# Performance work log

Measured on AMD Instinct MI355X. Metric: run time of the kernel, lower is better.

## Reference

```python
import jax, jax.numpy as jnp
import numpy as np

T, B, D_IN, H, V = 512, 128, 1024, 128, 4
NH, HD, MAXLEN = 4, 32, 64  # 4 heads * 32 = embed_dim 128; MAX_LENGTH=64


def _cell(pre, h, c, Whh):
    # pre = x @ W_ih.T + b, computed by caller. PyTorch gate order: i, f, g, o.
    g = pre + h @ Whh.T
    i, f, gg, o = jnp.split(g, 4, axis=-1)
    c = jax.nn.sigmoid(f) * c + jax.nn.sigmoid(i) * jnp.tanh(gg)
    h = jax.nn.sigmoid(o) * jnp.tanh(c)
    return h, c


def _lstm_layer(xs, Wih, Whh, b):
    # xs: [T, B, D]; input GEMM hoisted out of the scan as one big matmul
    pre = xs @ Wih.T + b  # [T, B, 4H]
    z = jnp.zeros((xs.shape[1], Whh.shape[1]), xs.dtype)

    def step(carry, p):
        h, c = carry
        h, c = _cell(p, h, c, Whh)
        return (h, c), h

    _, hs = jax.lax.scan(step, (z, z), pre)
    return hs  # [T, B, H]


def setup_inputs() -> dict:
    key = jax.random.key(0)
    ks = jax.random.split(key, 23)
    s = 0.08

    def rn(k, shape):
        return jax.random.normal(k, shape, jnp.float32) * s

    return {
        "x": jax.random.normal(ks[0], (T, B, D_IN), jnp.float32),
        "enc_Wih0": rn(ks[1], (4 * H, D_IN)), "enc_Whh0": rn(ks[2], (4 * H, H)), "enc_b0": rn(ks[3], (4 * H,)),
        "enc_Wih1": rn(ks[4], (4 * H, H)), "enc_Whh1": rn(ks[5], (4 * H, H)), "enc_b1": rn(ks[6], (4 * H,)),
        "dec_Wih0": rn(ks[7], (4 * H, H + V)), "dec_Whh0": rn(ks[8], (4 * H, H)), "dec_b0": rn(ks[9], (4 * H,)),
        "dec_Wih1": rn(ks[10], (4 * H, H)), "dec_Whh1": rn(ks[11], (4 * H, H)), "dec_b1": rn(ks[12], (4 * H,)),
        "Wq": rn(ks[13], (H, H)), "bq": rn(ks[14], (H,)),
        "Wk": rn(ks[15], (H, H)), "bk": rn(ks[16], (H,)),
        "Wv": rn(ks[17], (H, H)), "bv": rn(ks[18], (H,)),
        "Wo": rn(ks[19], (H, H)), "bo": rn(ks[20], (H,)),
        "lin_W": rn(ks[21], (V, 2 * H)), "lin_b": rn(ks[22], (V,)),
    }


def reference(x, enc_Wih0, enc_Whh0, enc_b0, enc_Wih1, enc_Whh1, enc_b1,
              dec_Wih0, dec_Whh0, dec_b0, dec_Wih1, dec_Whh1, dec_b1,
              Wq, bq, Wk, bk, Wv, bv, Wo, bo, lin_W, lin_b):
    # 2-layer encoder LSTM over the CNN feature sequence
    enc = _lstm_layer(_lstm_layer(x, enc_Wih0, enc_Whh0, enc_b0),
                      enc_Wih1, enc_Whh1, enc_b1)  # [T, B, H]

    # K/V projections of the (fixed) encoding hoisted out of the decode loop
    k = (enc @ Wk.T + bk).reshape(T, B, NH, HD)
    v = (enc @ Wv.T + bv).reshape(T, B, NH, HD)
    scale = 1.0 / float(np.sqrt(HD))

    z = jnp.zeros((B, H), x.dtype)

    def step(carry, _):
        h0, c0, h1, c1, y, ct = carry
        xin = jnp.concatenate([y, ct], axis=-1)  # cat([y, c_t]) -> [B, V+H]
        h0, c0 = _cell(xin @ dec_Wih0.T + dec_b0, h0, c0, dec_Whh0)
        h1, c1 = _cell(h0 @ dec_Wih1.T + dec_b1, h1, c1, dec_Whh1)
        s1 = h1  # top-layer LSTM output, query of length 1
        q = (s1 @ Wq.T + bq).reshape(B, NH, HD)
        attn = jax.nn.softmax(jnp.einsum('bhd,tbhd->bht', q, k) * scale, axis=-1)
        ct = jnp.einsum('bht,tbhd->bhd', attn, v).reshape(B, H) @ Wo.T + bo
        y = jnp.concatenate([s1, ct], axis=-1) @ lin_W.T + lin_b  # [B, V]
        return (h0, c0, h1, c1, y, ct), y

    init = (z, z, z, z, jnp.zeros((B, V), x.dtype), z)
    _, ys = jax.lax.scan(step, init, None, length=MAXLEN)
    return ys  # [MAX_LENGTH, B, V]
```

## Files before the change

### kernel.cpp

```cpp
#include <hip/hip_runtime.h>
#include <hip/hip_bf16.h>

typedef __attribute__((ext_vector_type(8))) short s16x8;
typedef __attribute__((ext_vector_type(4))) float f32x4;

__device__ inline unsigned short f2bf(float f) {
  unsigned u = __builtin_bit_cast(unsigned, f);
  unsigned r = (u + 0x7FFFu + ((u >> 16) & 1u)) >> 16;
  return (unsigned short)r;
}
__device__ inline float bf2f(short v) {
  return __builtin_bit_cast(float, ((unsigned)(unsigned short)v) << 16);
}
__device__ inline float bflo(unsigned w) { return __builtin_bit_cast(float, w << 16); }
__device__ inline float bfhi(unsigned w) { return __builtin_bit_cast(float, w & 0xFFFF0000u); }
__device__ inline float sigf(float x) { return 1.f / (1.f + __expf(-x)); }
__device__ inline float tanhf_(float x) { float e = __expf(2.f * x); return 1.f - 2.f / (e + 1.f); }

__global__ void packT(const float* __restrict__ src, unsigned* __restrict__ dst,
                      int rows, int scols, int kkPairs) {
  int i = blockIdx.x * 256 + threadIdx.x;
  if (i >= kkPairs * rows) return;
  int kk = i / rows, o = i % rows;
  int k0 = 2 * kk, k1 = 2 * kk + 1;
  float lo = (k0 < scols) ? src[(size_t)o * scols + k0] : 0.f;
  float hi = (k1 < scols) ? src[(size_t)o * scols + k1] : 0.f;
  dst[i] = (unsigned)f2bf(lo) | ((unsigned)f2bf(hi) << 16);
}
__global__ void packTg(const float* __restrict__ src, unsigned* __restrict__ dst,
                       int scols, int kkPairs) {
  int i = blockIdx.x * 256 + threadIdx.x;
  if (i >= kkPairs * 512) return;
  int kk = i / 512, j = i % 512;
  int row = (j & 3) * 128 + (j >> 2);
  int k0 = 2 * kk, k1 = 2 * kk + 1;
  float lo = (k0 < scols) ? src[(size_t)row * scols + k0] : 0.f;
  float hi = (k1 < scols) ? src[(size_t)row * scols + k1] : 0.f;
  dst[i] = (unsigned)f2bf(lo) | ((unsigned)f2bf(hi) << 16);
}
__global__ void f2bf_vec(const float* __restrict__ src, unsigned short* __restrict__ dst) {
  size_t i = ((size_t)blockIdx.x * 256 + threadIdx.x) * 4;
  float4 v = *(const float4*)(src + i);
  ushort4 o;
  o.x = f2bf(v.x); o.y = f2bf(v.y); o.z = f2bf(v.z); o.w = f2bf(v.w);
  *(ushort4*)(dst + i) = o;
}

#define BM 128
#define BN 128
#define BKK 32

template<int A_BF16, int C_BF16>
__global__ __launch_bounds__(256) void gemm_bt(const void* __restrict__ Av,
    const float* __restrict__ B, const float* __restrict__ bias,
    void* __restrict__ Cv, int M, int N, int K) {
  __shared__ short sA[BM * BKK];
  __shared__ short sB[BN * BKK];
  const int tid = threadIdx.x;
  const int l = tid & 63;
  const int wid = tid >> 6;
  const int wr = wid >> 1, wc = wid & 1;
  const int lr = l & 15, kg = l >> 4;
  const int bn = blockIdx.x, bm = blockIdx.y;
  const int arow = tid >> 1;
  const int acol = (tid & 1) * 16;

  f32x4 acc[4][4];
#pragma unroll
  for (int i = 0; i < 4; ++i)
#pragma unroll
    for (int j = 0; j < 4; ++j) acc[i][j] = (f32x4){0.f, 0.f, 0.f, 0.f};

  for (int kt = 0; kt < K; kt += BKK) {
    __syncthreads();
    if (A_BF16) {
      const unsigned short* src = (const unsigned short*)Av + (size_t)(bm * BM + arow) * K + kt + acol;
      *(s16x8*)&sA[arow * BKK + acol] = *(const s16x8*)src;
      *(s16x8*)&sA[arow * BKK + acol + 8] = *(const s16x8*)(src + 8);
    } else {
      const float* src = (const float*)Av + (size_t)(bm * BM + arow) * K + kt + acol;
      s16x8 v0, v1;
#pragma unroll
      for (int e = 0; e < 8; ++e) { v0[e] = (short)f2bf(src[e]); v1[e] = (short)f2bf(src[8 + e]); }
      *(s16x8*)&sA[arow * BKK + acol] = v0;
      *(s16x8*)&sA[arow * BKK + acol + 8] = v1;
    }
    {
      const float* src = B + (size_t)(bn * BN + arow) * K + kt + acol;
      s16x8 v0, v1;
#pragma unroll
      for (int e = 0; e < 8; ++e) { v0[e] = (short)f2bf(src[e]); v1[e] = (short)f2bf(src[8 + e]); }
      *(s16x8*)&sB[arow * BKK + acol] = v0;
      *(s16x8*)&sB[arow * BKK + acol + 8] = v1;
    }
    __syncthreads();
    s16x8 af[4], bfr[4];
#pragma unroll
    for (int mi = 0; mi < 4; ++mi)
      af[mi] = *(const s16x8*)&sA[(wr * 64 + mi * 16 + lr) * BKK + kg * 8];
#pragma unroll
    for (int ni = 0; ni < 4; ++ni)
      bfr[ni] = *(const s16x8*)&sB[(wc * 64 + ni * 16 + lr) * BKK + kg * 8];
#pragma unroll
    for (int mi = 0; mi < 4; ++mi)
#pragma unroll
      for (int ni = 0; ni < 4; ++ni)
        acc[mi][ni] = __builtin_amdgcn_mfma_f32_16x16x32_bf16(af[mi], bfr[ni], acc[mi][ni], 0, 0, 0);
  }
  const int r0 = bm * BM + wr * 64;
  const int c0 = bn * BN + wc * 64;
#pragma unroll
  for (int mi = 0; mi < 4; ++mi)
#pragma unroll
    for (int ni = 0; ni < 4; ++ni) {
      const int col = c0 + ni * 16 + lr;
      const float bv = bias[col];
#pragma unroll
      for (int e = 0; e < 4; ++e) {
        const int row = r0 + mi * 16 + kg * 4 + e;
        const float v = acc[mi][ni][e] + bv;
        if (C_BF16) ((unsigned short*)Cv)[(size_t)row * N + col] = f2bf(v);
        else        ((float*)Cv)[(size_t)row * N + col] = v;
      }
    }
}

__global__ __launch_bounds__(512) void lstm_scan(const float* __restrict__ pre,
    const float* __restrict__ Whh, unsigned short* __restrict__ hs, int T) {
  __shared__ unsigned short hb[2][2048];
  const int tid = threadIdx.x;
  const int l = tid & 63, w = tid >> 6;
  const int wg = blockIdx.x;
  const int lr = l & 15, kg = l >> 4;
  const int col = w * 16 + lr;
  const int rbase = kg * 4;

  s16x8 wf[4][4];
#pragma unroll
  for (int gi = 0; gi < 4; ++gi)
#pragma unroll
    for (int kk = 0; kk < 4; ++kk) {
      const float* p = Whh + (size_t)(gi * 128 + col) * 128 + kk * 32 + kg * 8;
#pragma unroll
      for (int e = 0; e < 8; ++e) wf[gi][kk][e] = (short)f2bf(p[e]);
    }
  for (int i = tid; i < 4096; i += 512) ((unsigned short*)hb)[i] = 0;
  float c[4] = {0.f, 0.f, 0.f, 0.f};

  const float* pbase = pre + ((size_t)(wg * 16 + rbase)) * 512 + col;
  float pf[16];
#pragma unroll
  for (int gi = 0; gi < 4; ++gi)
#pragma unroll
    for (int e = 0; e < 4; ++e) pf[gi * 4 + e] = pbase[e * 512 + gi * 128];
  __syncthreads();

  for (int t = 0; t < T; ++t) {
    const unsigned short* hc = hb[t & 1];
    unsigned short* hn = hb[(t & 1) ^ 1];
    s16x8 a[4];
#pragma unroll
    for (int kk = 0; kk < 4; ++kk) {
      const int byt = lr * 256 + ((kk * 64 + kg * 16) ^ ((lr & 7) << 4));
      a[kk] = *(const s16x8*)((const char*)hc + byt);
    }
    f32x4 acc[4];
#pragma unroll
    for (int gi = 0; gi < 4; ++gi)
      acc[gi] = (f32x4){pf[gi * 4], pf[gi * 4 + 1], pf[gi * 4 + 2], pf[gi * 4 + 3]};
    float pfn[16];
    if (t + 1 < T) {
      const float* pb2 = pbase + (size_t)(t + 1) * 65536;
#pragma unroll
      for (int gi = 0; gi < 4; ++gi)
#pragma unroll
        for (int e = 0; e < 4; ++e) pfn[gi * 4 + e] = pb2[e * 512 + gi * 128];
    } else {
#pragma unroll
      for (int i2 = 0; i2 < 16; ++i2) pfn[i2] = 0.f;
    }
#pragma unroll
    for (int kk = 0; kk < 4; ++kk)
#pragma unroll
      for (int gi = 0; gi < 4; ++gi)
        acc[gi] = __builtin_amdgcn_mfma_f32_16x16x32_bf16(a[kk], wf[gi][kk], acc[gi], 0, 0, 0);
#pragma unroll
    for (int e = 0; e < 4; ++e) {
      float gi_ = sigf(acc[0][e]);
      float gf  = sigf(acc[1][e]);
      float gg  = tanhf_(acc[2][e]);
      float go  = sigf(acc[3][e]);
      c[e] = gf * c[e] + gi_ * gg;
      float h = go * tanhf_(c[e]);
      unsigned short hu = f2bf(h);
      int row = rbase + e;
      int byt = row * 256 + ((col * 2) ^ ((row & 7) << 4));
      *(unsigned short*)((char*)hn + byt) = hu;
      hs[((size_t)t * 128 + wg * 16 + row) * 128 + col] = hu;
    }
#pragma unroll
    for (int i2 = 0; i2 < 16; ++i2) pf[i2] = pfn[i2];
    __syncthreads();
  }
}


#define DEC_SMEM 147200

__global__ void __launch_bounds__(512, 1) decoder_single(
    const unsigned short* __restrict__ kb, const unsigned short* __restrict__ vb,
    const unsigned* __restrict__ w0t,  const unsigned* __restrict__ wh0t,
    const unsigned* __restrict__ wi1t, const unsigned* __restrict__ wh1t,
    const unsigned* __restrict__ wqt,  const unsigned* __restrict__ wot,
    const float* __restrict__ b0, const float* __restrict__ b1,
    const float* __restrict__ bq, const float* __restrict__ bo,
    const float* __restrict__ linW, const float* __restrict__ linb,
    float* __restrict__ out)
{
  extern __shared__ char smem[];
  unsigned short* Kl = (unsigned short*)smem;
  float* xin = (float*)(smem + 131072);
  float* h0p = (float*)(smem + 131648);
  float* h1p = (float*)(smem + 132672);
  float* qx  = (float*)(smem + 133696);
  float* ctv = (float*)(smem + 134208);
  float* sc  = (float*)(smem + 134720);
  float* avp = (float*)(smem + 142912);
  float* part= (float*)(smem + 144960);
  float* red = (float*)(smem + 147008);
  float* isl = (float*)(smem + 147136);

  const int b = blockIdx.x;
  const int tid = threadIdx.x;
  const int l = tid & 63, wv = tid >> 6;
  const int lb = l & ~3;
  const int gate = tid & 3, o512 = tid >> 2;
  const int o128 = tid & 127, qd = tid >> 7;

  {
    const unsigned* kb32 = (const unsigned*)kb;
#pragma unroll
    for (int it = 0; it < 64; ++it) {
      const int i = tid + it * 512;
      const int t = i >> 6, c32 = i & 63;
      const unsigned v = kb32[(size_t)t * 8192 + b * 64 + c32];
      const int slot = c32 >> 2, w32 = c32 & 3;
      *(unsigned*)((char*)Kl + t * 256 + (((slot + t) & 15) << 4) + w32 * 4) = v;
    }
  }
  const float b0r = b0[gate * 128 + o512];
  const float b1r = b1[gate * 128 + o512];
  const float bqr = bq[o128];
  const float bor = bo[o128];
  float cc0 = 0.f, cc1 = 0.f;

  if (tid < 136) xin[tid] = 0.f;
  if (tid < 128) { h0p[tid] = 0.f; h0p[128 + tid] = 0.f; h1p[tid] = 0.f; h1p[128 + tid] = 0.f; }
  __syncthreads();

  const float scale = 0.1767766952966369f;

  for (int s = 0; s < 64; ++s) {
    const float* h0c = h0p + (s & 1) * 128;
    float* h0n = h0p + ((s & 1) ^ 1) * 128;
    const float* h1c = h1p + (s & 1) * 128;
    float* h1n = h1p + ((s & 1) ^ 1) * 128;

    {
      float a0 = b0r, a1 = 0.f;
      const unsigned* wp = w0t + tid;
#pragma unroll 8
      for (int kk = 0; kk < 68; ++kk) {
        const unsigned w2 = wp[kk * 512];
        const float2 x2 = *(const float2*)(xin + 2 * kk);
        a0 += x2.x * bflo(w2); a1 += x2.y * bfhi(w2);
      }
      const unsigned* hp = wh0t + tid;
#pragma unroll 8
      for (int kk = 0; kk < 64; ++kk) {
        const unsigned w2 = hp[kk * 512];
        const float2 h2 = *(const float2*)(h0c + 2 * kk);
        a0 += h2.x * bflo(w2); a1 += h2.y * bfhi(w2);
      }
      const float gval = a0 + a1;
      const float iv = __shfl(gval, lb + 0);
      const float fv = __shfl(gval, lb + 1);
      const float gv = __shfl(gval, lb + 2);
      const float ov = __shfl(gval, lb + 3);
      cc0 = sigf(fv) * cc0 + sigf(iv) * tanhf_(gv);
      const float h = sigf(ov) * tanhf_(cc0);
      if (gate == 0) h0n[o512] = h;
    }
    __syncthreads();
    {
      float a0 = b1r, a1 = 0.f;
      const unsigned* ip = wi1t + tid;
      const unsigned* hp = wh1t + tid;
#pragma unroll 8
      for (int kk = 0; kk < 64; ++kk) {
        const unsigned wa = ip[kk * 512];
        const unsigned wb = hp[kk * 512];
        const float2 a2 = *(const float2*)(h0n + 2 * kk);
        const float2 b2 = *(const float2*)(h1c + 2 * kk);
        a0 += a2.x * bflo(wa) + b2.x * bflo(wb);
        a1 += a2.y * bfhi(wa) + b2.y * bfhi(wb);
      }
      const float gval = a0 + a1;
      const float iv = __shfl(gval, lb + 0);
      const float fv = __shfl(gval, lb + 1);
      const float gv = __shfl(gval, lb + 2);
      const float ov = __shfl(gval, lb + 3);
      cc1 = sigf(fv) * cc1 + sigf(iv) * tanhf_(gv);
      const float h = sigf(ov) * tanhf_(cc1);
      if (gate == 0) h1n[o512] = h;
    }
    __syncthreads();
    {
      float a0 = 0.f, a1 = 0.f;
      const unsigned* wp = wqt + (size_t)(qd * 16) * 128 + o128;
#pragma unroll
      for (int m = 0; m < 16; ++m) {
        const unsigned w2 = wp[(size_t)m * 128];
        const float2 h2 = *(const float2*)(h1n + qd * 32 + 2 * m);
        a0 += h2.x * bflo(w2);
        a1 += h2.y * bfhi(w2);
      }
      part[qd * 128 + o128] = a0 + a1;
    }
    __syncthreads();
    if (tid < 128)
      qx[tid] = (bqr + part[tid] + part[128 + tid] + part[256 + tid] + part[384 + tid]) * scale;
    __syncthreads();
    {
      const int t = tid;
      float s0 = 0.f, s1 = 0.f, s2 = 0.f, s3 = 0.f;
      const char* krow = (const char*)Kl + t * 256;
#pragma unroll
      for (int c = 0; c < 16; ++c) {
        const s16x8 kv = *(const s16x8*)(krow + (((c + t) & 15) << 4));
        const f32x4 qA = *(const f32x4*)(qx + c * 8);
        const f32x4 qB = *(const f32x4*)(qx + c * 8 + 4);
        float d = qA[0] * bf2f(kv[0]) + qA[1] * bf2f(kv[1]) + qA[2] * bf2f(kv[2]) + qA[3] * bf2f(kv[3])
                + qB[0] * bf2f(kv[4]) + qB[1] * bf2f(kv[5]) + qB[2] * bf2f(kv[6]) + qB[3] * bf2f(kv[7]);
        if ((c >> 2) == 0) s0 += d; else if ((c >> 2) == 1) s1 += d; else if ((c >> 2) == 2) s2 += d; else s3 += d;
      }
      float p0 = __expf(s0), p1 = __expf(s1), p2 = __expf(s2), p3 = __expf(s3);
      sc[0 * 512 + t] = p0; sc[1 * 512 + t] = p1; sc[2 * 512 + t] = p2; sc[3 * 512 + t] = p3;
#pragma unroll
      for (int off = 32; off > 0; off >>= 1) {
        p0 += __shfl_xor(p0, off); p1 += __shfl_xor(p1, off);
        p2 += __shfl_xor(p2, off); p3 += __shfl_xor(p3, off);
      }
      if (l == 0) { red[0 + wv] = p0; red[8 + wv] = p1; red[16 + wv] = p2; red[24 + wv] = p3; }
    }
    __syncthreads();
    if (tid < 4) {
      float sm = red[tid * 8];
#pragma unroll
      for (int w2 = 1; w2 < 8; ++w2) sm += red[tid * 8 + w2];
      isl[tid] = 1.f / sm;
    }
    {
      const int d = tid & 127, tc = tid >> 7, h = d >> 5;
      const unsigned short* vp = vb + (size_t)(tc * 128) * 16384 + (size_t)b * 128 + d;
      const float* scp = sc + h * 512 + tc * 128;
      float acc = 0.f;
#pragma unroll 8
      for (int tt = 0; tt < 128; ++tt)
        acc += scp[tt] * bf2f((short)vp[(size_t)tt * 16384]);
      avp[tc * 128 + d] = acc;
    }
    __syncthreads();
    if (tid < 128)
      ctv[tid] = (avp[tid] + avp[128 + tid] + avp[256 + tid] + avp[384 + tid]) * isl[tid >> 5];
    __syncthreads();
    {
      float a0 = 0.f, a1 = 0.f;
      const unsigned* wp = wot + (size_t)(qd * 16) * 128 + o128;
#pragma unroll
      for (int m = 0; m < 16; ++m) {
        const unsigned w2 = wp[(size_t)m * 128];
        const float2 c2 = *(const float2*)(ctv + qd * 32 + 2 * m);
        a0 += c2.x * bflo(w2);
        a1 += c2.y * bfhi(w2);
      }
      part[qd * 128 + o128] = a0 + a1;
    }
    __syncthreads();
    if (tid < 128)
      xin[4 + tid] = bor + part[tid] + part[128 + tid] + part[256 + tid] + part[384 + tid];
    __syncthreads();
    if (tid < 256) {
      const int o = tid >> 6, j = tid & 63;
      const float* lw = linW + o * 256;
      float p = h1n[j] * lw[j] + h1n[j + 64] * lw[j + 64]
              + xin[4 + j] * lw[128 + j] + xin[4 + j + 64] * lw[192 + j];
#pragma unroll
      for (int off = 32; off > 0; off >>= 1) p += __shfl_xor(p, off);
      if (j == 0) {
        const float yv = p + linb[o];
        out[((size_t)s * 128 + b) * 4 + o] = yv;
        xin[o] = yv;
      }
    }
    __syncthreads();
  }
}

extern "C" void kernel_launch(void* const* d_in, const int* in_sizes, int n_in,
                              void* d_out, int out_size, void* d_ws, size_t ws_size,
                              hipStream_t stream) {
  (void)in_sizes; (void)n_in; (void)out_size;
  const float* x     = (const float*)d_in[0];
  const float* eWih0 = (const float*)d_in[1];
  const float* eWhh0 = (const float*)d_in[2];
  const float* eb0   = (const float*)d_in[3];
  const float* eWih1 = (const float*)d_in[4];
  const float* eWhh1 = (const float*)d_in[5];
  const float* eb1   = (const float*)d_in[6];
  const float* dWih0 = (const float*)d_in[7];
  const float* dWhh0 = (const float*)d_in[8];
  const float* db0   = (const float*)d_in[9];
  const float* dWih1 = (const float*)d_in[10];
  const float* dWhh1 = (const float*)d_in[11];
  const float* db1   = (const float*)d_in[12];
  const float* Wq    = (const float*)d_in[13];
  const float* bq    = (const float*)d_in[14];
  const float* Wk    = (const float*)d_in[15];
  const float* bk    = (const float*)d_in[16];
  const float* Wv    = (const float*)d_in[17];
  const float* bv    = (const float*)d_in[18];
  const float* Wo    = (const float*)d_in[19];
  const float* bo    = (const float*)d_in[20];
  const float* linW  = (const float*)d_in[21];
  const float* linb  = (const float*)d_in[22];

  char* w = (char*)d_ws;
  float* pre  = (float*)(w + 524288);
  size_t off = 524288 + (size_t)65536 * 512 * 4;
  unsigned short* hs0  = (unsigned short*)(w + off); off += (size_t)65536 * 128 * 2;
  unsigned short* enc  = (unsigned short*)(w + off); off += (size_t)65536 * 128 * 2;
  unsigned short* kbuf = (unsigned short*)(w + off); off += (size_t)65536 * 128 * 2;
  unsigned short* vbuf = (unsigned short*)(w + off); off += (size_t)65536 * 128 * 2;
  unsigned* w0t  = (unsigned*)(w + off); off += (size_t)68 * 512 * 4;
  unsigned* wh0t = (unsigned*)(w + off); off += (size_t)64 * 512 * 4;
  unsigned* wi1t = (unsigned*)(w + off); off += (size_t)64 * 512 * 4;
  unsigned* wh1t = (unsigned*)(w + off); off += (size_t)64 * 512 * 4;
  unsigned* wqt  = (unsigned*)(w + off); off += (size_t)64 * 128 * 4;
  unsigned* wot  = (unsigned*)(w + off); off += (size_t)64 * 128 * 4;
  unsigned short* xbf = (unsigned short*)(w + off);
  const size_t need_big = off + (size_t)65536 * 1024 * 2;
  const bool big = ws_size >= need_big;

  packTg<<<(68 * 512 + 255) / 256, 256, 0, stream>>>(dWih0, w0t, 132, 68);
  packTg<<<(64 * 512 + 255) / 256, 256, 0, stream>>>(dWhh0, wh0t, 128, 64);
  packTg<<<(64 * 512 + 255) / 256, 256, 0, stream>>>(dWih1, wi1t, 128, 64);
  packTg<<<(64 * 512 + 255) / 256, 256, 0, stream>>>(dWhh1, wh1t, 128, 64);
  packT<<<(64 * 128 + 255) / 256, 256, 0, stream>>>(Wq, wqt, 128, 128, 64);
  packT<<<(64 * 128 + 255) / 256, 256, 0, stream>>>(Wo, wot, 128, 128, 64);

  if (big) {
    f2bf_vec<<<65536, 256, 0, stream>>>(x, xbf);
    gemm_bt<1, 0><<<dim3(4, 512), 256, 0, stream>>>((const void*)xbf, eWih0, eb0, (void*)pre, 65536, 512, 1024);
  } else {
    gemm_bt<0, 0><<<dim3(4, 512), 256, 0, stream>>>((const void*)x, eWih0, eb0, (void*)pre, 65536, 512, 1024);
  }
  lstm_scan<<<8, 512, 0, stream>>>(pre, eWhh0, hs0, 512);
  gemm_bt<1, 0><<<dim3(4, 512), 256, 0, stream>>>((const void*)hs0, eWih1, eb1, (void*)pre, 65536, 512, 128);
  lstm_scan<<<8, 512, 0, stream>>>(pre, eWhh1, enc, 512);
  gemm_bt<1, 1><<<dim3(1, 512), 256, 0, stream>>>((const void*)enc, Wk, bk, (void*)kbuf, 65536, 128, 128);
  gemm_bt<1, 1><<<dim3(1, 512), 256, 0, stream>>>((const void*)enc, Wv, bv, (void*)vbuf, 65536, 128, 128);

  hipFuncSetAttribute((const void*)decoder_single,
                      hipFuncAttributeMaxDynamicSharedMemorySize, DEC_SMEM);
  decoder_single<<<128, 512, DEC_SMEM, stream>>>(kbuf, vbuf, w0t, wh0t, wi1t, wh1t, wqt, wot,
      db0, db1, bq, bo, linW, linb, (float*)d_out);
}
```

Baseline: 3.645 ms.

## Fold Wo into output linear, shuffle-reduce decoder projections, bf16 layer-1 preactivations

Precomputes linW_ctx·Wo and the combined bias on device, so the decoder's output head reads the attention context directly and no longer waits on the Wo projection. The Wq/Wo projections now reduce across four lanes with shuffles instead of shared-memory partials and extra barriers. The layer-1 input GEMM writes bf16 preactivations that the second LSTM scan reads, halving that traffic. In exchange it adds a small setup kernel, costs some precision in the preactivations, and changes the summation order.

```diff
diff --git a/kernel.cpp b/kernel.cpp
--- a/kernel.cpp
+++ b/kernel.cpp
@@ -44,6 +44,20 @@
   ushort4 o;
   o.x = f2bf(v.x); o.y = f2bf(v.y); o.z = f2bf(v.z); o.w = f2bf(v.w);
   *(ushort4*)(dst + i) = o;
+}
+__global__ void foldWo(const float* __restrict__ linW, const float* __restrict__ Wo,
+                       const float* __restrict__ bo, const float* __restrict__ linb,
+                       float* __restrict__ lwcWo, float* __restrict__ linb2) {
+  const int tid = threadIdx.x;
+  const int o4 = tid >> 7, k = tid & 127;
+  float acc = 0.f;
+  for (int j = 0; j < 128; ++j) acc += linW[o4 * 256 + 128 + j] * Wo[(size_t)j * 128 + k];
+  lwcWo[o4 * 128 + k] = acc;
+  if (k == 0) {
+    float a2 = linb[o4];
+    for (int j = 0; j < 128; ++j) a2 += linW[o4 * 256 + 128 + j] * bo[j];
+    linb2[o4] = a2;
+  }
 }
 
 #define BM 128
@@ -125,7 +139,8 @@
     }
 }
 
-__global__ __launch_bounds__(512) void lstm_scan(const float* __restrict__ pre,
+template<int PRE_BF16>
+__global__ __launch_bounds__(512) void lstm_scan(const void* __restrict__ prev,
     const float* __restrict__ Whh, unsigned short* __restrict__ hs, int T) {
   __shared__ unsigned short hb[2][2048];
   const int tid = threadIdx.x;
@@ -147,12 +162,15 @@
   for (int i = tid; i < 4096; i += 512) ((unsigned short*)hb)[i] = 0;
   float c[4] = {0.f, 0.f, 0.f, 0.f};
 
-  const float* pbase = pre + ((size_t)(wg * 16 + rbase)) * 512 + col;
+  const size_t base = ((size_t)(wg * 16 + rbase)) * 512 + col;
+  const float* pf32 = (const float*)prev + base;
+  const unsigned short* pbf = (const unsigned short*)prev + base;
   float pf[16];
 #pragma unroll
   for (int gi = 0; gi < 4; ++gi)
 #pragma unroll
-    for (int e = 0; e < 4; ++e) pf[gi * 4 + e] = pbase[e * 512 + gi * 128];
+    for (int e = 0; e < 4; ++e)
+      pf[gi * 4 + e] = PRE_BF16 ? bf2f((short)pbf[e * 512 + gi * 128]) : pf32[e * 512 + gi * 128];
   __syncthreads();
 
   for (int t = 0; t < T; ++t) {
@@ -170,11 +188,13 @@
       acc[gi] = (f32x4){pf[gi * 4], pf[gi * 4 + 1], pf[gi * 4 + 2], pf[gi * 4 + 3]};
     float pfn[16];
     if (t + 1 < T) {
-      const float* pb2 = pbase + (size_t)(t + 1) * 65536;
+      const size_t ofs = (size_t)(t + 1) * 65536;
 #pragma unroll
       for (int gi = 0; gi < 4; ++gi)
 #pragma unroll
-        for (int e = 0; e < 4; ++e) pfn[gi * 4 + e] = pb2[e * 512 + gi * 128];
+        for (int e = 0; e < 4; ++e)
+          pfn[gi * 4 + e] = PRE_BF16 ? bf2f((short)pbf[ofs + e * 512 + gi * 128])
+                                     : pf32[ofs + e * 512 + gi * 128];
     } else {
 #pragma unroll
       for (int i2 = 0; i2 < 16; ++i2) pfn[i2] = 0.f;
@@ -205,7 +225,7 @@
 }
 
 
-#define DEC_SMEM 147200
+#define DEC_SMEM 148736
 
 __global__ void __launch_bounds__(512, 1) decoder_single(
     const unsigned short* __restrict__ kb, const unsigned short* __restrict__ vb,
@@ -214,27 +234,29 @@
     const unsigned* __restrict__ wqt,  const unsigned* __restrict__ wot,
     const float* __restrict__ b0, const float* __restrict__ b1,
     const float* __restrict__ bq, const float* __restrict__ bo,
-    const float* __restrict__ linW, const float* __restrict__ linb,
-    float* __restrict__ out)
+    const float* __restrict__ linW, const float* __restrict__ lwcWo,
+    const float* __restrict__ linb2, float* __restrict__ out)
 {
   extern __shared__ char smem[];
   unsigned short* Kl = (unsigned short*)smem;
-  float* xin = (float*)(smem + 131072);
-  float* h0p = (float*)(smem + 131648);
-  float* h1p = (float*)(smem + 132672);
-  float* qx  = (float*)(smem + 133696);
-  float* ctv = (float*)(smem + 134208);
-  float* sc  = (float*)(smem + 134720);
-  float* avp = (float*)(smem + 142912);
-  float* part= (float*)(smem + 144960);
-  float* red = (float*)(smem + 147008);
-  float* isl = (float*)(smem + 147136);
+  float* xin  = (float*)(smem + 131072);
+  float* h0p  = (float*)(smem + 131648);
+  float* h1p  = (float*)(smem + 132672);
+  float* qx   = (float*)(smem + 133696);
+  float* sc   = (float*)(smem + 134208);
+  float* avpT = (float*)(smem + 142400);
+  float* red  = (float*)(smem + 144448);
+  float* isl  = (float*)(smem + 144576);
+  float* linWhL  = (float*)(smem + 144592);
+  float* lwcWoL  = (float*)(smem + 146640);
+  float* linb2L  = (float*)(smem + 148688);
 
   const int b = blockIdx.x;
   const int tid = threadIdx.x;
   const int l = tid & 63, wv = tid >> 6;
   const int lb = l & ~3;
   const int gate = tid & 3, o512 = tid >> 2;
+  const int oq = tid >> 2, kq = tid & 3;
   const int o128 = tid & 127, qd = tid >> 7;
 
   {
@@ -250,12 +272,17 @@
   }
   const float b0r = b0[gate * 128 + o512];
   const float b1r = b1[gate * 128 + o512];
-  const float bqr = bq[o128];
-  const float bor = bo[o128];
+  const float bqv = bq[oq];
+  const float bov = bo[oq];
   float cc0 = 0.f, cc1 = 0.f;
 
   if (tid < 136) xin[tid] = 0.f;
   if (tid < 128) { h0p[tid] = 0.f; h0p[128 + tid] = 0.f; h1p[tid] = 0.f; h1p[128 + tid] = 0.f; }
+  {
+    linWhL[tid & 511] = linW[(size_t)(tid >> 7) * 256 + (tid & 127)];
+    lwcWoL[tid & 511] = lwcWo[tid];
+    if (tid < 4) linb2L[tid] = linb2[tid];
+  }
   __syncthreads();
 
   const float scale = 0.1767766952966369f;
@@ -317,19 +344,19 @@
     __syncthreads();
     {
       float a0 = 0.f, a1 = 0.f;
-      const unsigned* wp = wqt + (size_t)(qd * 16) * 128 + o128;
+      const unsigned* wp = wqt + (size_t)(kq * 16) * 128 + oq;
 #pragma unroll
       for (int m = 0; m < 16; ++m) {
         const unsigned w2 = wp[(size_t)m * 128];
-        const float2 h2 = *(const float2*)(h1n + qd * 32 + 2 * m);
+        const float2 h2 = *(const float2*)(h1n + kq * 32 + 2 * m);
         a0 += h2.x * bflo(w2);
         a1 += h2.y * bfhi(w2);
       }
-      part[qd * 128 + o128] = a0 + a1;
-    }
-    __syncthreads();
-    if (tid < 128)
-      qx[tid] = (bqr + part[tid] + part[128 + tid] + part[256 + tid] + part[384 + tid]) * scale;
+      float p = a0 + a1;
+      p += __shfl_xor(p, 1);
+      p += __shfl_xor(p, 2);
+      if (kq == 0) qx[oq] = (bqv + p) * scale;
+    }
     __syncthreads();
     {
       const int t = tid;
@@ -368,40 +395,43 @@
 #pragma unroll 8
       for (int tt = 0; tt < 128; ++tt)
         acc += scp[tt] * bf2f((short)vp[(size_t)tt * 16384]);
-      avp[tc * 128 + d] = acc;
-    }
-    __syncthreads();
-    if (tid < 128)
-      ctv[tid] = (avp[tid] + avp[128 + tid] + avp[256 + tid] + avp[384 + tid]) * isl[tid >> 5];
-    __syncthreads();
-    {
+      avpT[d * 4 + tc] = acc;
+    }
+    __syncthreads();
+    {
+      const float iq = isl[kq];
       float a0 = 0.f, a1 = 0.f;
-      const unsigned* wp = wot + (size_t)(qd * 16) * 128 + o128;
+      const unsigned* wp = wot + (size_t)(kq * 16) * 128 + oq;
 #pragma unroll
       for (int m = 0; m < 16; ++m) {
         const unsigned w2 = wp[(size_t)m * 128];
-        const float2 c2 = *(const float2*)(ctv + qd * 32 + 2 * m);
-        a0 += c2.x * bflo(w2);
-        a1 += c2.y * bfhi(w2);
-      }
-      part[qd * 128 + o128] = a0 + a1;
-    }
-    __syncthreads();
-    if (tid < 128)
-      xin[4 + tid] = bor + part[tid] + part[128 + tid] + part[256 + tid] + part[384 + tid];
-    __syncthreads();
-    if (tid < 256) {
-      const int o = tid >> 6, j = tid & 63;
-      const float* lw = linW + o * 256;
-      float p = h1n[j] * lw[j] + h1n[j + 64] * lw[j + 64]
-              + xin[4 + j] * lw[128 + j] + xin[4 + j + 64] * lw[192 + j];
+        const int k2 = kq * 32 + 2 * m;
+        const f32x4 vA = *(const f32x4*)(avpT + k2 * 4);
+        const f32x4 vB = *(const f32x4*)(avpT + (k2 + 1) * 4);
+        const float c0v = (vA[0] + vA[1] + vA[2] + vA[3]) * iq;
+        const float c1v = (vB[0] + vB[1] + vB[2] + vB[3]) * iq;
+        a0 += c0v * bflo(w2);
+        a1 += c1v * bfhi(w2);
+      }
+      float p = a0 + a1;
+      p += __shfl_xor(p, 1);
+      p += __shfl_xor(p, 2);
+      if (kq == 0) xin[4 + oq] = bov + p;
+    }
+    {
+      const int j = o128;
+      const f32x4 vA = *(const f32x4*)(avpT + j * 4);
+      const float ctvj = (vA[0] + vA[1] + vA[2] + vA[3]) * isl[j >> 5];
+      float p = h1n[j] * linWhL[qd * 128 + j] + ctvj * lwcWoL[qd * 128 + j];
 #pragma unroll
       for (int off = 32; off > 0; off >>= 1) p += __shfl_xor(p, off);
-      if (j == 0) {
-        const float yv = p + linb[o];
-        out[((size_t)s * 128 + b) * 4 + o] = yv;
-        xin[o] = yv;
-      }
+      if (l == 0) red[wv] = p;
+    }
+    __syncthreads();
+    if (tid < 4) {
+      const float yv = red[2 * tid] + red[2 * tid + 1] + linb2L[tid];
+      out[((size_t)s * 128 + b) * 4 + tid] = yv;
+      xin[tid] = yv;
     }
     __syncthreads();
   }
@@ -448,6 +478,8 @@
   unsigned* wh1t = (unsigned*)(w + off); off += (size_t)64 * 512 * 4;
   unsigned* wqt  = (unsigned*)(w + off); off += (size_t)64 * 128 * 4;
   unsigned* wot  = (unsigned*)(w + off); off += (size_t)64 * 128 * 4;
+  float* lwcWo   = (float*)(w + off);    off += 4 * 128 * 4;
+  float* linb2   = (float*)(w + off);    off += 64;
   unsigned short* xbf = (unsigned short*)(w + off);
   const size_t need_big = off + (size_t)65536 * 1024 * 2;
   const bool big = ws_size >= need_big;
@@ -458,6 +490,7 @@
   packTg<<<(64 * 512 + 255) / 256, 256, 0, stream>>>(dWhh1, wh1t, 128, 64);
   packT<<<(64 * 128 + 255) / 256, 256, 0, stream>>>(Wq, wqt, 128, 128, 64);
   packT<<<(64 * 128 + 255) / 256, 256, 0, stream>>>(Wo, wot, 128, 128, 64);
+  foldWo<<<1, 512, 0, stream>>>(linW, Wo, bo, linb, lwcWo, linb2);
 
   if (big) {
     f2bf_vec<<<65536, 256, 0, stream>>>(x, xbf);
@@ -465,14 +498,14 @@
   } else {
     gemm_bt<0, 0><<<dim3(4, 512), 256, 0, stream>>>((const void*)x, eWih0, eb0, (void*)pre, 65536, 512, 1024);
   }
-  lstm_scan<<<8, 512, 0, stream>>>(pre, eWhh0, hs0, 512);
-  gemm_bt<1, 0><<<dim3(4, 512), 256, 0, stream>>>((const void*)hs0, eWih1, eb1, (void*)pre, 65536, 512, 128);
-  lstm_scan<<<8, 512, 0, stream>>>(pre, eWhh1, enc, 512);
+  lstm_scan<0><<<8, 512, 0, stream>>>((const void*)pre, eWhh0, hs0, 512);
+  gemm_bt<1, 1><<<dim3(4, 512), 256, 0, stream>>>((const void*)hs0, eWih1, eb1, (void*)pre, 65536, 512, 128);
+  lstm_scan<1><<<8, 512, 0, stream>>>((const void*)pre, eWhh1, enc, 512);
   gemm_bt<1, 1><<<dim3(1, 512), 256, 0, stream>>>((const void*)enc, Wk, bk, (void*)kbuf, 65536, 128, 128);
   gemm_bt<1, 1><<<dim3(1, 512), 256, 0, stream>>>((const void*)enc, Wv, bv, (void*)vbuf, 65536, 128, 128);
 
   hipFuncSetAttribute((const void*)decoder_single,
                       hipFuncAttributeMaxDynamicSharedMemorySize, DEC_SMEM);
   decoder_single<<<128, 512, DEC_SMEM, stream>>>(kbuf, vbuf, w0t, wh0t, wi1t, wh1t, wqt, wot,
-      db0, db1, bq, bo, linW, linb, (float*)d_out);
-}
+      db0, db1, bq, bo, linW, lwcWo, linb2, (float*)d_out);
+}
```

Measured after the change: 3.725 ms. 1.02x slower.
